# Performance work log

Hardware: AMD Instinct MI355X
Metric: run time of the kernel (lower is better)

Reference implementation:

```python
import jax, jax.numpy as jnp
import numpy as np

N_NODES = 100000
NEG_SLOPE = 0.2


def gat_conv(x, W, att_src, att_dst, bias, src, dst, heads, out_ch):
    # x: [N, F_in]; W: [F_in, heads*out_ch]; att_*: [heads, out_ch]; bias: [heads*out_ch]
    N = x.shape[0]
    h = (x @ W).reshape(N, heads, out_ch)                 # [N, H, C]
    a_src = jnp.sum(h * att_src[None], axis=-1)           # [N, H]
    a_dst = jnp.sum(h * att_dst[None], axis=-1)           # [N, H]
    # per-edge unnormalized attention logits (PyG GATConv)
    alpha = jax.nn.leaky_relu(a_src[src] + a_dst[dst], NEG_SLOPE)   # [E, H]
    # scatter-softmax over edges grouped by destination node
    m = jax.ops.segment_max(alpha, dst, num_segments=N)   # [N, H]
    m = jnp.where(jnp.isfinite(m), m, 0.0)
    e = jnp.exp(alpha - m[dst])                           # [E, H]
    s = jax.ops.segment_sum(e, dst, num_segments=N)       # [N, H]
    alpha = e / (s[dst] + 1e-16)
    # weighted scatter-add aggregation of neighbor features
    out = jax.ops.segment_sum(alpha[:, :, None] * h[src], dst, num_segments=N)  # [N, H, C]
    return out.reshape(N, heads * out_ch) + bias


def setup_inputs() -> dict:
    key = jax.random.key(0)
    ks = jax.random.split(key, 10)
    F_in = 128
    x = jax.random.normal(ks[0], (N_NODES, F_in), dtype=jnp.float32)
    edge_index = jax.random.randint(ks[1], (2, 3200000), 0, N_NODES, dtype=jnp.int64)
    g = 0.1
    return {
        "x": x,
        "edge_index": edge_index,
        "W1": jax.random.normal(ks[2], (F_in, 32), jnp.float32) * g,
        "att_src1": jax.random.normal(ks[3], (2, 16), jnp.float32) * g,
        "att_dst1": jax.random.normal(ks[4], (2, 16), jnp.float32) * g,
        "b1": jnp.zeros((32,), jnp.float32),
        "W2": jax.random.normal(ks[5], (32, 2), jnp.float32) * g,
        "att_src2": jax.random.normal(ks[6], (1, 2), jnp.float32) * g,
        "att_dst2": jax.random.normal(ks[7], (1, 2), jnp.float32) * g,
        "b2": jnp.zeros((2,), jnp.float32),
    }


def reference(x, edge_index, W1, att_src1, att_dst1, b1, W2, att_src2, att_dst2, b2):
    N = x.shape[0]
    # add self-loops (PyG GATConv default add_self_loops=True)
    loops = jnp.arange(N, dtype=edge_index.dtype)
    src = jnp.concatenate([edge_index[0], loops])
    dst = jnp.concatenate([edge_index[1], loops])
    h = gat_conv(x, W1, att_src1, att_dst1, b1, src, dst, heads=2, out_ch=16)
    h = jax.nn.elu(h)
    h = gat_conv(h, W2, att_src2, att_dst2, b2, src, dst, heads=1, out_ch=2)
    return jax.nn.log_softmax(h, axis=1)
```

## Files before the change

### kernel.cpp

```cpp
#include <hip/hip_runtime.h>
#include <hip/hip_bf16.h>
#include <hip/hip_fp16.h>

#define LEAK   0.2f
#define NPB    200
#define CAP    8192
#define CAPSH  13
#define SBITS  17
#define SMASK  0x1FFFF
#define CHUNKB 8192

__device__ __forceinline__ unsigned pkh(float a, float b) {
    __half2 h = __floats2half2_rn(a, b);
    return *(unsigned*)&h;
}
__device__ __forceinline__ float2 uph(unsigned u) {
    __half2 h = *(__half2*)&u;
    return __half22float2(h);
}

__global__ __launch_bounds__(512) void kbin(const int* __restrict__ ei, int E, int K,
                                            int* __restrict__ cursor,
                                            int* __restrict__ binned) {
    __shared__ int hist[512], gb[512], lc[512];
    __shared__ int probe;
    int t = threadIdx.x;
    hist[t] = 0;
    if (t == 0) probe = 0;
    __syncthreads();
    if (t < 256) {
        int zc = 0;
#pragma unroll
        for (int j = 0; j < 4; j++) zc += (ei[(t * 4 + j) * 2 + 1] == 0) ? 1 : 0;
        if (zc) atomicAdd(&probe, zc);
    }
    __syncthreads();
    int f = (probe == 1024);
    int e0 = blockIdx.x * CHUNKB;
    int ss[16], dd[16];
#pragma unroll
    for (int i = 0; i < 16; i++) {
        int e = e0 + t + 512 * i;
        ss[i] = -1;
        dd[i] = 0;
        if (e < E) {
            int s, d;
            if (f) { s = ei[2 * e]; d = ei[2 * (e + E)]; }
            else   { s = ei[e];     d = ei[e + E]; }
            ss[i] = s;
            dd[i] = d;
            atomicAdd(&hist[d / NPB], 1);
        }
    }
    __syncthreads();
    int h = hist[t];
    lc[t] = 0;
    if (t < K && h) gb[t] = (t << CAPSH) + atomicAdd(&cursor[t], h);
    __syncthreads();
#pragma unroll
    for (int i = 0; i < 16; i++) {
        if (ss[i] >= 0) {
            int bk = dd[i] / NPB;
            int dloc = dd[i] - bk * NPB;
            int pos = atomicAdd(&lc[bk], 1);
            int gpos = gb[bk] + pos;
            if (gpos < ((bk + 1) << CAPSH))
                binned[gpos] = ss[i] | (dloc << SBITS);
        }
    }
}

__global__ __launch_bounds__(256) void k1(const float* __restrict__ x,
                                          const float* __restrict__ W1,
                                          const float* __restrict__ atts,
                                          const float* __restrict__ attd,
                                          uint2* __restrict__ h1h,
                                          float* __restrict__ a1s,
                                          float* __restrict__ a1d, int N) {
    __shared__ float Ws[128 * 32];
    __shared__ float xs[64 * 132];
    int t = threadIdx.x;
    const float4* W4 = (const float4*)W1;
    float4* Ws4 = (float4*)Ws;
#pragma unroll
    for (int i = 0; i < 4; i++) Ws4[t + 256 * i] = W4[t + 256 * i];
    long long node0 = (long long)blockIdx.x * 64;
    const float4* x4 = (const float4*)x;
    float4* xs4 = (float4*)xs;
#pragma unroll
    for (int i = 0; i < 8; i++) {
        int idx = t + 256 * i;
        int row = idx >> 5, col = idx & 31;
        long long n = node0 + row;
        float4 v = make_float4(0.f, 0.f, 0.f, 0.f);
        if (n < N) v = x4[n * 32 + col];
        xs4[row * 33 + col] = v;
    }
    __syncthreads();

    int cg = t & 7, ns = t >> 3;
    const float4* xr0 = (const float4*)(xs + (ns * 2) * 132);
    const float4* xr1 = (const float4*)(xs + (ns * 2 + 1) * 132);
    float acc0[4] = {0.f, 0.f, 0.f, 0.f}, acc1[4] = {0.f, 0.f, 0.f, 0.f};
#pragma unroll 8
    for (int k4 = 0; k4 < 32; k4++) {
        float4 xa = xr0[k4], xb = xr1[k4];
        float av[4] = {xa.x, xa.y, xa.z, xa.w};
        float bv[4] = {xb.x, xb.y, xb.z, xb.w};
#pragma unroll
        for (int i = 0; i < 4; i++) {
            float4 w = Ws4[(k4 * 4 + i) * 8 + cg];
            acc0[0] = fmaf(av[i], w.x, acc0[0]);
            acc0[1] = fmaf(av[i], w.y, acc0[1]);
            acc0[2] = fmaf(av[i], w.z, acc0[2]);
            acc0[3] = fmaf(av[i], w.w, acc0[3]);
            acc1[0] = fmaf(bv[i], w.x, acc1[0]);
            acc1[1] = fmaf(bv[i], w.y, acc1[1]);
            acc1[2] = fmaf(bv[i], w.z, acc1[2]);
            acc1[3] = fmaf(bv[i], w.w, acc1[3]);
        }
    }
    long long gn0 = node0 + ns * 2, gn1 = gn0 + 1;
    if (gn0 < N) h1h[gn0 * 8 + cg] = make_uint2(pkh(acc0[0], acc0[1]),
                                                pkh(acc0[2], acc0[3]));
    if (gn1 < N) h1h[gn1 * 8 + cg] = make_uint2(pkh(acc1[0], acc1[1]),
                                                pkh(acc1[2], acc1[3]));

    float ps0 = 0.f, pd0 = 0.f, ps1 = 0.f, pd1 = 0.f;
#pragma unroll
    for (int i = 0; i < 4; i++) {
        float aa = atts[cg * 4 + i], dd = attd[cg * 4 + i];
        ps0 = fmaf(acc0[i], aa, ps0);
        pd0 = fmaf(acc0[i], dd, pd0);
        ps1 = fmaf(acc1[i], aa, ps1);
        pd1 = fmaf(acc1[i], dd, pd1);
    }
#pragma unroll
    for (int m = 1; m < 4; m <<= 1) {
        ps0 += __shfl_xor(ps0, m, 64);
        pd0 += __shfl_xor(pd0, m, 64);
        ps1 += __shfl_xor(ps1, m, 64);
        pd1 += __shfl_xor(pd1, m, 64);
    }
    if ((cg & 3) == 0) {
        int hd = cg >> 2;
        if (gn0 < N) { a1s[gn0 * 2 + hd] = ps0; a1d[gn0 * 2 + hd] = pd0; }
        if (gn1 < N) { a1s[gn1 * 2 + hd] = ps1; a1d[gn1 * 2 + hd] = pd1; }
    }
}

__global__ __launch_bounds__(1024) void kfused(const int* __restrict__ cursor,
                                               const int* __restrict__ binned,
                                               const uint2* __restrict__ h1h,
                                               const float* __restrict__ a1s,
                                               const float* __restrict__ a1d,
                                               const float* __restrict__ b1,
                                               const float* __restrict__ W2,
                                               const float* __restrict__ as2,
                                               const float* __restrict__ ad2,
                                               float4* __restrict__ pk,
                                               int* __restrict__ srcs,
                                               int* __restrict__ od, int N) {
    __shared__ int lsrc[CAP];
    __shared__ int ldeg[NPB], lcur[NPB], loff[NPB];
    __shared__ int swt[4];
    int b = blockIdx.x, t = threadIdx.x;
    int node0 = b * NPB;
    int nn = min(NPB, N - node0);
    int cnt = cursor[b];
    if (cnt > CAP) cnt = CAP;
    const int* bb = binned + ((long long)b << CAPSH);
    if (t < NPB) ldeg[t] = 0;
    __syncthreads();
    int pv[8];
#pragma unroll
    for (int j = 0; j < 8; j++) {
        int i = t + 1024 * j;
        pv[j] = (i < cnt) ? bb[i] : -1;
        if (pv[j] >= 0) atomicAdd(&ldeg[pv[j] >> SBITS], 1);
    }
    __syncthreads();
    {
        int v = 0, xsc = 0;
        if (t < 256) {
            v = (t < nn) ? ldeg[t] : 0;
            xsc = v;
#pragma unroll
            for (int o = 1; o < 64; o <<= 1) {
                int y = __shfl_up(xsc, o, 64);
                if ((t & 63) >= o) xsc += y;
            }
            if ((t & 63) == 63) swt[t >> 6] = xsc;
        }
        __syncthreads();
        if (t < 256) {
            int add = 0;
#pragma unroll
            for (int j = 0; j < 4; j++)
                if (j < (t >> 6)) add += swt[j];
            xsc += add;
            if (t < nn) {
                int rel = xsc - v;
                loff[t] = rel;
                lcur[t] = rel;
                od[node0 + t] = rel | (v << 14);
            }
        }
        __syncthreads();
    }
#pragma unroll
    for (int j = 0; j < 8; j++) {
        if (pv[j] >= 0) {
            int pos = atomicAdd(&lcur[pv[j] >> SBITS], 1);
            lsrc[pos] = pv[j] & SMASK;
        }
    }
    __syncthreads();
    for (int i = t; i < cnt; i += 1024) srcs[((long long)b << CAPSH) + i] = lsrc[i];

    int wv = t >> 6, lane = t & 63;
    int e8 = lane >> 3, c4 = lane & 7, hd = c4 >> 2;
    bool wlane = (c4 & 3) == 0;
    for (int ni = wv; ni < nn; ni += 16) {
        int n = node0 + ni;
        float a1dn = a1d[2 * n + hd];
        int base = loff[ni], g = ldeg[ni];
        float4 acc = make_float4(0.f, 0.f, 0.f, 0.f);
        float wsum = 0.f;
        for (int tt = e8 - 1; tt < g; tt += 8) {
            int s = (tt < 0) ? n : lsrc[base + tt];
            float al = a1s[2 * s + hd] + a1dn;
            al = al > 0.f ? al : LEAK * al;
            float w = __expf(al);
            uint2 hb = h1h[(size_t)s * 8 + c4];
            float2 f01 = uph(hb.x), f23 = uph(hb.y);
            acc.x = fmaf(w, f01.x, acc.x);
            acc.y = fmaf(w, f01.y, acc.y);
            acc.z = fmaf(w, f23.x, acc.z);
            acc.w = fmaf(w, f23.y, acc.w);
            if (wlane) wsum += w;
        }
#pragma unroll
        for (int m = 8; m < 64; m <<= 1) {
            acc.x += __shfl_xor(acc.x, m, 64);
            acc.y += __shfl_xor(acc.y, m, 64);
            acc.z += __shfl_xor(acc.z, m, 64);
            acc.w += __shfl_xor(acc.w, m, 64);
            wsum += __shfl_xor(wsum, m, 64);
        }
        float wsH = __shfl(wsum, hd * 4, 64);
        float inv = 1.f / (wsH + 1e-16f);
        float4 bv = ((const float4*)b1)[c4];
        float4 t1;
        t1.x = acc.x * inv + bv.x;
        t1.y = acc.y * inv + bv.y;
        t1.z = acc.z * inv + bv.z;
        t1.w = acc.w * inv + bv.w;
        t1.x = t1.x > 0.f ? t1.x : __expf(t1.x) - 1.f;
        t1.y = t1.y > 0.f ? t1.y : __expf(t1.y) - 1.f;
        t1.z = t1.z > 0.f ? t1.z : __expf(t1.z) - 1.f;
        t1.w = t1.w > 0.f ? t1.w : __expf(t1.w) - 1.f;
        const float4* W24 = (const float4*)W2;
        float4 wA = W24[c4 * 2], wB = W24[c4 * 2 + 1];
        float p0 = t1.x * wA.x + t1.y * wA.z + t1.z * wB.x + t1.w * wB.z;
        float p1 = t1.x * wA.y + t1.y * wA.w + t1.z * wB.y + t1.w * wB.w;
#pragma unroll
        for (int m = 1; m < 8; m <<= 1) {
            p0 += __shfl_xor(p0, m, 64);
            p1 += __shfl_xor(p1, m, 64);
        }
        if (lane == 0)
            pk[n] = make_float4(p0 * as2[0] + p1 * as2[1], p0, p1,
                                p0 * ad2[0] + p1 * ad2[1]);
    }
}

__global__ __launch_bounds__(256) void kagg2(const int* __restrict__ od,
                                             const int* __restrict__ srcs,
                                             const float4* __restrict__ pk,
                                             const float* __restrict__ b2,
                                             float* __restrict__ out, int N) {
    int sub = threadIdx.x >> 5, k = threadIdx.x & 31;
    int n = blockIdx.x * 8 + sub;
    if (n >= N) return;
    float4 pn = pk[n];
    float adn = pn.w;
    int o = od[n];
    int base = ((n / NPB) << CAPSH) + (o & 16383);
    int g = o >> 14;
    float a0 = 0.f, a1v = 0.f, wsm = 0.f;
    for (int e = k - 1; e < g; e += 32) {
        float4 p = (e < 0) ? pn : pk[srcs[base + e]];
        float al = p.x + adn;
        al = al > 0.f ? al : LEAK * al;
        float w = __expf(al);
        a0 = fmaf(w, p.y, a0);
        a1v = fmaf(w, p.z, a1v);
        wsm += w;
    }
#pragma unroll
    for (int m = 1; m < 32; m <<= 1) {
        a0 += __shfl_xor(a0, m, 32);
        a1v += __shfl_xor(a1v, m, 32);
        wsm += __shfl_xor(wsm, m, 32);
    }
    if (k == 0) {
        float inv = 1.f / (wsm + 1e-16f);
        float o0 = a0 * inv + b2[0];
        float o1 = a1v * inv + b2[1];
        float mx = fmaxf(o0, o1);
        float lse = mx + __logf(__expf(o0 - mx) + __expf(o1 - mx));
        ((float2*)out)[n] = make_float2(o0 - lse, o1 - lse);
    }
}

extern "C" void kernel_launch(void* const* d_in, const int* in_sizes, int n_in,
                              void* d_out, int out_size, void* d_ws, size_t ws_size,
                              hipStream_t stream) {
    const float* x   = (const float*)d_in[0];
    const int*   ei  = (const int*)d_in[1];
    const float* W1  = (const float*)d_in[2];
    const float* as1 = (const float*)d_in[3];
    const float* ad1 = (const float*)d_in[4];
    const float* b1  = (const float*)d_in[5];
    const float* W2  = (const float*)d_in[6];
    const float* as2 = (const float*)d_in[7];
    const float* ad2 = (const float*)d_in[8];
    const float* b2  = (const float*)d_in[9];
    float* out = (float*)d_out;

    int N = out_size / 2;
    int E = in_sizes[1] / 2;
    int K = (N + NPB - 1) / NPB;

    float* wsp   = (float*)d_ws;
    float4* pk   = (float4*)wsp;
    uint2* h1h   = (uint2*)(pk + (size_t)N);
    float* a1s   = (float*)(h1h + (size_t)N * 8);
    float* a1d   = a1s + (size_t)N * 2;
    int* od      = (int*)(a1d + (size_t)N * 2);
    int* srcs    = od + N;
    int* binned  = srcs + (size_t)K * CAP;
    int* cursor  = binned + (size_t)K * CAP;

    int nblkB = (E + CHUNKB - 1) / CHUNKB;

    hipMemsetAsync(cursor, 0, K * sizeof(int), stream);
    kbin<<<nblkB, 512, 0, stream>>>(ei, E, K, cursor, binned);
    k1<<<(N + 63) / 64, 256, 0, stream>>>(x, W1, as1, ad1, h1h, a1s, a1d, N);
    kfused<<<K, 1024, 0, stream>>>(cursor, binned, h1h, a1s, a1d,
                                   b1, W2, as2, ad2, pk, srcs, od, N);
    kagg2<<<(N + 7) / 8, 256, 0, stream>>>(od, srcs, pk, b2, out, N);
}
```

Measured before the change: 239.4 us.

## Merge binning with layer-1 projection and fuse layer-2 aggregation via cooperative grid sync

```diff
diff --git a/kernel.cpp b/kernel.cpp
--- a/kernel.cpp
+++ b/kernel.cpp
@@ -1,6 +1,9 @@
 #include <hip/hip_runtime.h>
 #include <hip/hip_bf16.h>
 #include <hip/hip_fp16.h>
+#include <hip/hip_cooperative_groups.h>
+
+namespace cg = cooperative_groups;
 
 #define LEAK   0.2f
 #define NPB    200
@@ -19,148 +22,159 @@
     return __half22float2(h);
 }
 
-__global__ __launch_bounds__(512) void kbin(const int* __restrict__ ei, int E, int K,
+__global__ __launch_bounds__(256) void kpre(const int* __restrict__ ei, int E, int K,
+                                            int NBIN,
                                             int* __restrict__ cursor,
-                                            int* __restrict__ binned) {
-    __shared__ int hist[512], gb[512], lc[512];
-    __shared__ int probe;
-    int t = threadIdx.x;
-    hist[t] = 0;
-    if (t == 0) probe = 0;
-    __syncthreads();
-    if (t < 256) {
-        int zc = 0;
-#pragma unroll
-        for (int j = 0; j < 4; j++) zc += (ei[(t * 4 + j) * 2 + 1] == 0) ? 1 : 0;
-        if (zc) atomicAdd(&probe, zc);
-    }
-    __syncthreads();
-    int f = (probe == 1024);
-    int e0 = blockIdx.x * CHUNKB;
-    int ss[16], dd[16];
-#pragma unroll
-    for (int i = 0; i < 16; i++) {
-        int e = e0 + t + 512 * i;
-        ss[i] = -1;
-        dd[i] = 0;
-        if (e < E) {
-            int s, d;
-            if (f) { s = ei[2 * e]; d = ei[2 * (e + E)]; }
-            else   { s = ei[e];     d = ei[e + E]; }
-            ss[i] = s;
-            dd[i] = d;
-            atomicAdd(&hist[d / NPB], 1);
-        }
-    }
-    __syncthreads();
-    int h = hist[t];
-    lc[t] = 0;
-    if (t < K && h) gb[t] = (t << CAPSH) + atomicAdd(&cursor[t], h);
-    __syncthreads();
-#pragma unroll
-    for (int i = 0; i < 16; i++) {
-        if (ss[i] >= 0) {
-            int bk = dd[i] / NPB;
-            int dloc = dd[i] - bk * NPB;
-            int pos = atomicAdd(&lc[bk], 1);
-            int gpos = gb[bk] + pos;
-            if (gpos < ((bk + 1) << CAPSH))
-                binned[gpos] = ss[i] | (dloc << SBITS);
-        }
-    }
-}
-
-__global__ __launch_bounds__(256) void k1(const float* __restrict__ x,
-                                          const float* __restrict__ W1,
-                                          const float* __restrict__ atts,
-                                          const float* __restrict__ attd,
-                                          uint2* __restrict__ h1h,
-                                          float* __restrict__ a1s,
-                                          float* __restrict__ a1d, int N) {
+                                            int* __restrict__ binned,
+                                            const float* __restrict__ x,
+                                            const float* __restrict__ W1,
+                                            const float* __restrict__ atts,
+                                            const float* __restrict__ attd,
+                                            uint2* __restrict__ h1h,
+                                            float* __restrict__ a1s,
+                                            float* __restrict__ a1d, int N) {
     __shared__ float Ws[128 * 32];
     __shared__ float xs[64 * 132];
     int t = threadIdx.x;
-    const float4* W4 = (const float4*)W1;
-    float4* Ws4 = (float4*)Ws;
-#pragma unroll
-    for (int i = 0; i < 4; i++) Ws4[t + 256 * i] = W4[t + 256 * i];
-    long long node0 = (long long)blockIdx.x * 64;
-    const float4* x4 = (const float4*)x;
-    float4* xs4 = (float4*)xs;
-#pragma unroll
-    for (int i = 0; i < 8; i++) {
-        int idx = t + 256 * i;
-        int row = idx >> 5, col = idx & 31;
-        long long n = node0 + row;
-        float4 v = make_float4(0.f, 0.f, 0.f, 0.f);
-        if (n < N) v = x4[n * 32 + col];
-        xs4[row * 33 + col] = v;
-    }
-    __syncthreads();
-
-    int cg = t & 7, ns = t >> 3;
-    const float4* xr0 = (const float4*)(xs + (ns * 2) * 132);
-    const float4* xr1 = (const float4*)(xs + (ns * 2 + 1) * 132);
-    float acc0[4] = {0.f, 0.f, 0.f, 0.f}, acc1[4] = {0.f, 0.f, 0.f, 0.f};
+
+    if (blockIdx.x < NBIN) {
+        int* hist = (int*)xs;
+        int* gb   = hist + 512;
+        int* lc   = gb + 512;
+        int* pr   = lc + 512;
+        hist[t] = 0;
+        hist[t + 256] = 0;
+        if (t == 0) *pr = 0;
+        __syncthreads();
+        {
+            int zc = 0;
+#pragma unroll
+            for (int j = 0; j < 4; j++) zc += (ei[(t * 4 + j) * 2 + 1] == 0) ? 1 : 0;
+            if (zc) atomicAdd(pr, zc);
+        }
+        __syncthreads();
+        int f = (*pr == 1024);
+        int e0 = blockIdx.x * CHUNKB;
+        int ss[32], dd[32];
+#pragma unroll
+        for (int i = 0; i < 32; i++) {
+            int e = e0 + t + 256 * i;
+            ss[i] = -1;
+            dd[i] = 0;
+            if (e < E) {
+                int s, d;
+                if (f) { s = ei[2 * e]; d = ei[2 * (e + E)]; }
+                else   { s = ei[e];     d = ei[e + E]; }
+                ss[i] = s;
+                dd[i] = d;
+                atomicAdd(&hist[d / NPB], 1);
+            }
+        }
+        __syncthreads();
+        for (int u = t; u < 512; u += 256) {
+            lc[u] = 0;
+            int h = hist[u];
+            if (u < K && h) gb[u] = (u << CAPSH) + atomicAdd(&cursor[u], h);
+        }
+        __syncthreads();
+#pragma unroll
+        for (int i = 0; i < 32; i++) {
+            if (ss[i] >= 0) {
+                int bk = dd[i] / NPB;
+                int dloc = dd[i] - bk * NPB;
+                int pos = atomicAdd(&lc[bk], 1);
+                int gpos = gb[bk] + pos;
+                if (gpos < ((bk + 1) << CAPSH))
+                    binned[gpos] = ss[i] | (dloc << SBITS);
+            }
+        }
+    } else {
+        int b = blockIdx.x - NBIN;
+        const float4* W4 = (const float4*)W1;
+        float4* Ws4 = (float4*)Ws;
+#pragma unroll
+        for (int i = 0; i < 4; i++) Ws4[t + 256 * i] = W4[t + 256 * i];
+        long long node0 = (long long)b * 64;
+        const float4* x4 = (const float4*)x;
+        float4* xs4 = (float4*)xs;
+#pragma unroll
+        for (int i = 0; i < 8; i++) {
+            int idx = t + 256 * i;
+            int row = idx >> 5, col = idx & 31;
+            long long n = node0 + row;
+            float4 v = make_float4(0.f, 0.f, 0.f, 0.f);
+            if (n < N) v = x4[n * 32 + col];
+            xs4[row * 33 + col] = v;
+        }
+        __syncthreads();
+
+        int cg_ = t & 7, ns = t >> 3;
+        const float4* xr0 = (const float4*)(xs + (ns * 2) * 132);
+        const float4* xr1 = (const float4*)(xs + (ns * 2 + 1) * 132);
+        float acc0[4] = {0.f, 0.f, 0.f, 0.f}, acc1[4] = {0.f, 0.f, 0.f, 0.f};
 #pragma unroll 8
-    for (int k4 = 0; k4 < 32; k4++) {
-        float4 xa = xr0[k4], xb = xr1[k4];
-        float av[4] = {xa.x, xa.y, xa.z, xa.w};
-        float bv[4] = {xb.x, xb.y, xb.z, xb.w};
+        for (int k4 = 0; k4 < 32; k4++) {
+            float4 xa = xr0[k4], xb = xr1[k4];
+            float av[4] = {xa.x, xa.y, xa.z, xa.w};
+            float bv[4] = {xb.x, xb.y, xb.z, xb.w};
+#pragma unroll
+            for (int i = 0; i < 4; i++) {
+                float4 w = Ws4[(k4 * 4 + i) * 8 + cg_];
+                acc0[0] = fmaf(av[i], w.x, acc0[0]);
+                acc0[1] = fmaf(av[i], w.y, acc0[1]);
+                acc0[2] = fmaf(av[i], w.z, acc0[2]);
+                acc0[3] = fmaf(av[i], w.w, acc0[3]);
+                acc1[0] = fmaf(bv[i], w.x, acc1[0]);
+                acc1[1] = fmaf(bv[i], w.y, acc1[1]);
+                acc1[2] = fmaf(bv[i], w.z, acc1[2]);
+                acc1[3] = fmaf(bv[i], w.w, acc1[3]);
+            }
+        }
+        long long gn0 = node0 + ns * 2, gn1 = gn0 + 1;
+        if (gn0 < N) h1h[gn0 * 8 + cg_] = make_uint2(pkh(acc0[0], acc0[1]),
+                                                     pkh(acc0[2], acc0[3]));
+        if (gn1 < N) h1h[gn1 * 8 + cg_] = make_uint2(pkh(acc1[0], acc1[1]),
+                                                     pkh(acc1[2], acc1[3]));
+
+        float ps0 = 0.f, pd0 = 0.f, ps1 = 0.f, pd1 = 0.f;
 #pragma unroll
         for (int i = 0; i < 4; i++) {
-            float4 w = Ws4[(k4 * 4 + i) * 8 + cg];
-            acc0[0] = fmaf(av[i], w.x, acc0[0]);
-            acc0[1] = fmaf(av[i], w.y, acc0[1]);
-            acc0[2] = fmaf(av[i], w.z, acc0[2]);
-            acc0[3] = fmaf(av[i], w.w, acc0[3]);
-            acc1[0] = fmaf(bv[i], w.x, acc1[0]);
-            acc1[1] = fmaf(bv[i], w.y, acc1[1]);
-            acc1[2] = fmaf(bv[i], w.z, acc1[2]);
-            acc1[3] = fmaf(bv[i], w.w, acc1[3]);
-        }
-    }
-    long long gn0 = node0 + ns * 2, gn1 = gn0 + 1;
-    if (gn0 < N) h1h[gn0 * 8 + cg] = make_uint2(pkh(acc0[0], acc0[1]),
-                                                pkh(acc0[2], acc0[3]));
-    if (gn1 < N) h1h[gn1 * 8 + cg] = make_uint2(pkh(acc1[0], acc1[1]),
-                                                pkh(acc1[2], acc1[3]));
-
-    float ps0 = 0.f, pd0 = 0.f, ps1 = 0.f, pd1 = 0.f;
-#pragma unroll
-    for (int i = 0; i < 4; i++) {
-        float aa = atts[cg * 4 + i], dd = attd[cg * 4 + i];
-        ps0 = fmaf(acc0[i], aa, ps0);
-        pd0 = fmaf(acc0[i], dd, pd0);
-        ps1 = fmaf(acc1[i], aa, ps1);
-        pd1 = fmaf(acc1[i], dd, pd1);
-    }
-#pragma unroll
-    for (int m = 1; m < 4; m <<= 1) {
-        ps0 += __shfl_xor(ps0, m, 64);
-        pd0 += __shfl_xor(pd0, m, 64);
-        ps1 += __shfl_xor(ps1, m, 64);
-        pd1 += __shfl_xor(pd1, m, 64);
-    }
-    if ((cg & 3) == 0) {
-        int hd = cg >> 2;
-        if (gn0 < N) { a1s[gn0 * 2 + hd] = ps0; a1d[gn0 * 2 + hd] = pd0; }
-        if (gn1 < N) { a1s[gn1 * 2 + hd] = ps1; a1d[gn1 * 2 + hd] = pd1; }
-    }
-}
-
-__global__ __launch_bounds__(1024) void kfused(const int* __restrict__ cursor,
-                                               const int* __restrict__ binned,
-                                               const uint2* __restrict__ h1h,
-                                               const float* __restrict__ a1s,
-                                               const float* __restrict__ a1d,
-                                               const float* __restrict__ b1,
-                                               const float* __restrict__ W2,
-                                               const float* __restrict__ as2,
-                                               const float* __restrict__ ad2,
-                                               float4* __restrict__ pk,
-                                               int* __restrict__ srcs,
-                                               int* __restrict__ od, int N) {
+            float aa = atts[cg_ * 4 + i], ddv = attd[cg_ * 4 + i];
+            ps0 = fmaf(acc0[i], aa, ps0);
+            pd0 = fmaf(acc0[i], ddv, pd0);
+            ps1 = fmaf(acc1[i], aa, ps1);
+            pd1 = fmaf(acc1[i], ddv, pd1);
+        }
+#pragma unroll
+        for (int m = 1; m < 4; m <<= 1) {
+            ps0 += __shfl_xor(ps0, m, 64);
+            pd0 += __shfl_xor(pd0, m, 64);
+            ps1 += __shfl_xor(ps1, m, 64);
+            pd1 += __shfl_xor(pd1, m, 64);
+        }
+        if ((cg_ & 3) == 0) {
+            int hd = cg_ >> 2;
+            if (gn0 < N) { a1s[gn0 * 2 + hd] = ps0; a1d[gn0 * 2 + hd] = pd0; }
+            if (gn1 < N) { a1s[gn1 * 2 + hd] = ps1; a1d[gn1 * 2 + hd] = pd1; }
+        }
+    }
+}
+
+template <int COOP>
+__global__ __launch_bounds__(1024, 8) void kmain(const int* __restrict__ cursor,
+                                                 const int* __restrict__ binned,
+                                                 const uint2* __restrict__ h1h,
+                                                 const float* __restrict__ a1s,
+                                                 const float* __restrict__ a1d,
+                                                 const float* __restrict__ b1,
+                                                 const float* __restrict__ W2,
+                                                 const float* __restrict__ as2,
+                                                 const float* __restrict__ ad2,
+                                                 float4* __restrict__ pk,
+                                                 const float* __restrict__ b2,
+                                                 float* __restrict__ out, int N,
+                                                 int* __restrict__ srcs,
+                                                 int* __restrict__ od) {
     __shared__ int lsrc[CAP];
     __shared__ int ldeg[NPB], lcur[NPB], loff[NPB];
     __shared__ int swt[4];
@@ -203,7 +217,7 @@
                 int rel = xsc - v;
                 loff[t] = rel;
                 lcur[t] = rel;
-                od[node0 + t] = rel | (v << 14);
+                if constexpr (!COOP) od[node0 + t] = rel | (v << 14);
             }
         }
         __syncthreads();
@@ -216,7 +230,9 @@
         }
     }
     __syncthreads();
-    for (int i = t; i < cnt; i += 1024) srcs[((long long)b << CAPSH) + i] = lsrc[i];
+    if constexpr (!COOP) {
+        for (int i = t; i < cnt; i += 1024) srcs[((long long)b << CAPSH) + i] = lsrc[i];
+    }
 
     int wv = t >> 6, lane = t & 63;
     int e8 = lane >> 3, c4 = lane & 7, hd = c4 >> 2;
@@ -272,6 +288,42 @@
         if (lane == 0)
             pk[n] = make_float4(p0 * as2[0] + p1 * as2[1], p0, p1,
                                 p0 * ad2[0] + p1 * ad2[1]);
+    }
+
+    if constexpr (COOP) {
+        __threadfence();
+        cg::this_grid().sync();
+        int sub = t >> 5, kk = t & 31;
+        for (int ni = sub; ni < nn; ni += 32) {
+            int n = node0 + ni;
+            float4 pn = pk[n];
+            float adn = pn.w;
+            int base = loff[ni], g = ldeg[ni];
+            float A0 = 0.f, A1 = 0.f, wsm = 0.f;
+            for (int e = kk - 1; e < g; e += 32) {
+                float4 p = (e < 0) ? pn : pk[lsrc[base + e]];
+                float al = p.x + adn;
+                al = al > 0.f ? al : LEAK * al;
+                float w = __expf(al);
+                A0 = fmaf(w, p.y, A0);
+                A1 = fmaf(w, p.z, A1);
+                wsm += w;
+            }
+#pragma unroll
+            for (int m = 1; m < 32; m <<= 1) {
+                A0 += __shfl_xor(A0, m, 32);
+                A1 += __shfl_xor(A1, m, 32);
+                wsm += __shfl_xor(wsm, m, 32);
+            }
+            if (kk == 0) {
+                float inv = 1.f / (wsm + 1e-16f);
+                float o0 = A0 * inv + b2[0];
+                float o1 = A1 * inv + b2[1];
+                float mx = fmaxf(o0, o1);
+                float lse = mx + __logf(__expf(o0 - mx) + __expf(o1 - mx));
+                ((float2*)out)[n] = make_float2(o0 - lse, o1 - lse);
+            }
+        }
     }
 }
 
@@ -343,12 +395,23 @@
     int* binned  = srcs + (size_t)K * CAP;
     int* cursor  = binned + (size_t)K * CAP;
 
-    int nblkB = (E + CHUNKB - 1) / CHUNKB;
+    int NBIN = (E + CHUNKB - 1) / CHUNKB;
+    int NK1  = (N + 63) / 64;
 
     hipMemsetAsync(cursor, 0, K * sizeof(int), stream);
-    kbin<<<nblkB, 512, 0, stream>>>(ei, E, K, cursor, binned);
-    k1<<<(N + 63) / 64, 256, 0, stream>>>(x, W1, as1, ad1, h1h, a1s, a1d, N);
-    kfused<<<K, 1024, 0, stream>>>(cursor, binned, h1h, a1s, a1d,
-                                   b1, W2, as2, ad2, pk, srcs, od, N);
-    kagg2<<<(N + 7) / 8, 256, 0, stream>>>(od, srcs, pk, b2, out, N);
-}
+    kpre<<<NBIN + NK1, 256, 0, stream>>>(ei, E, K, NBIN, cursor, binned,
+                                         x, W1, as1, ad1, h1h, a1s, a1d, N);
+
+    void* args[] = {(void*)&cursor, (void*)&binned, (void*)&h1h, (void*)&a1s,
+                    (void*)&a1d,    (void*)&b1,     (void*)&W2,  (void*)&as2,
+                    (void*)&ad2,    (void*)&pk,     (void*)&b2,  (void*)&out,
+                    (void*)&N,      (void*)&srcs,   (void*)&od};
+    hipError_t ce = hipLaunchCooperativeKernel((void*)kmain<1>, dim3(K), dim3(1024),
+                                               args, 0, stream);
+    if (ce != hipSuccess) {
+        (void)hipGetLastError();
+        kmain<0><<<K, 1024, 0, stream>>>(cursor, binned, h1h, a1s, a1d, b1, W2,
+                                         as2, ad2, pk, b2, out, N, srcs, od);
+        kagg2<<<(N + 7) / 8, 256, 0, stream>>>(od, srcs, pk, b2, out, N);
+    }
+}
```

Result: slower. 507.0 us (+111.7%).
